# Kernel optimization log

Measured on AMD Instinct MI355X. Metric: run time of the kernel, lower is better.

The kernel has to match this reference:

```python
import jax, jax.numpy as jnp
import numpy as np

N_HEAD, D_K, D_V, D_MODEL = 16, 64, 64, 1024
B, S = 2, 2048


def setup_inputs() -> dict:
    key = jax.random.key(0)
    ks = jax.random.split(key, 9)
    Q = jax.random.normal(ks[0], (B, S, D_MODEL), jnp.float32)
    K = jax.random.normal(ks[1], (B, S, D_MODEL), jnp.float32)
    V = jax.random.normal(ks[2], (B, S, D_MODEL), jnp.float32)
    mask = jax.random.randint(ks[3], (B, 1, S), 0, 2) > 0  # bool, ~half valid
    # xavier-normal-ish std for (d_model, d_k) fan
    std_qk = (2.0 / (D_MODEL + D_K)) ** 0.5
    std_v = (2.0 / (D_MODEL + D_V)) ** 0.5
    Wq = std_qk * jax.random.normal(ks[4], (N_HEAD, D_MODEL, D_K), jnp.float32)
    Wk = std_qk * jax.random.normal(ks[5], (N_HEAD, D_MODEL, D_K), jnp.float32)
    Wv = std_v * jax.random.normal(ks[6], (N_HEAD, D_MODEL, D_V), jnp.float32)
    bound = (6.0 / (N_HEAD * D_V)) ** 0.5  # kaiming_uniform-ish
    Wo = jax.random.uniform(ks[7], (N_HEAD * D_V, D_MODEL), jnp.float32, -bound, bound)
    return {"Q": Q, "K": K, "V": V, "Wq": Wq, "Wk": Wk, "Wv": Wv, "Wo": Wo, "mask": mask}


def reference(Q, K, V, Wq, Wk, Wv, Wo, mask):
    n_head, d_model, d_k = Wq.shape
    d_v = Wv.shape[-1]
    b, sq, _ = Q.shape
    sk = K.shape[1]
    # Per-head projections; torch cat over heads == leading head axis here.
    q = jnp.einsum('bsd,hdk->hbsk', Q, Wq)  # (H,B,Sq,dk)
    k = jnp.einsum('bsd,hdk->hbsk', K, Wk)  # (H,B,Sk,dk)
    v = jnp.einsum('bsd,hdv->hbsv', V, Wv)  # (H,B,Sk,dv)
    scores = jnp.einsum('hbqk,hbsk->hbqs', q, k) / (d_k ** 0.5)
    m = mask[None]  # (1,B,1,Sk), broadcasts over heads and queries
    scores = jnp.where(m, scores, -1e9)
    attn = jax.nn.softmax(scores, axis=-1)
    attn = jnp.where(m, attn, 0.0)
    out = jnp.einsum('hbqs,hbsv->hbqv', attn, v)  # (H,B,Sq,dv)
    # torch: split along batch*head dim then cat on feature dim -> head-major feature concat
    out = jnp.transpose(out, (1, 2, 0, 3)).reshape(b, sq, n_head * d_v)
    out = out @ Wo  # (B,Sq,d_model); dropout is identity in eval
    attns = attn.reshape(n_head * b, sq, sk)
    return out, attns
```

## Files before the change

### kernel.cpp

```cpp
#include <hip/hip_runtime.h>
#include <hip/hip_bf16.h>

typedef __attribute__((ext_vector_type(8))) short short8;
typedef __attribute__((ext_vector_type(4))) float floatx4;

#define H 16
#define BB 2
#define SS 2048
#define DM 1024
#define DK 64

__device__ __forceinline__ unsigned short f2bf(float f) {
  union { float f; unsigned int u; } x; x.f = f;
  unsigned int r = (x.u + 0x7fffu + ((x.u >> 16) & 1u)) >> 16;
  return (unsigned short)r;
}
__device__ __forceinline__ float bf2f(unsigned short h) {
  union { unsigned int u; float f; } x; x.u = (unsigned int)h << 16;
  return x.f;
}

__global__ __launch_bounds__(256) void convert_qkv(
    const float* __restrict__ Q, const float* __restrict__ K, const float* __restrict__ V,
    unsigned short* __restrict__ Qb, unsigned short* __restrict__ Kb,
    unsigned short* __restrict__ Vb) {
  const float* in; unsigned short* out;
  int z = blockIdx.y;
  if (z == 0)      { in = Q; out = Qb; }
  else if (z == 1) { in = K; out = Kb; }
  else             { in = V; out = Vb; }
  size_t i = ((size_t)blockIdx.x * 256 + threadIdx.x) * 4;
  float4 v = *(const float4*)&in[i];
  ushort4 o;
  o.x = f2bf(v.x); o.y = f2bf(v.y); o.z = f2bf(v.z); o.w = f2bf(v.w);
  *(ushort4*)&out[i] = o;
}

__global__ __launch_bounds__(256) void repack_w(
    const float* __restrict__ Wq, const float* __restrict__ Wk,
    const float* __restrict__ Wv, const float* __restrict__ Wo,
    unsigned short* __restrict__ Wq_t, unsigned short* __restrict__ Wk_t,
    unsigned short* __restrict__ Wv_t, unsigned short* __restrict__ Wo_t) {
  int z = blockIdx.z;
  int bx = blockIdx.x, by = blockIdx.y;
  int t = threadIdx.x;
  const float* in;
  unsigned short* out;
  if (z == 0)      { in = Wq; out = Wq_t; }
  else if (z == 1) { in = Wk; out = Wk_t; }
  else if (z == 2) { in = Wv; out = Wv_t; }
  else             { in = Wo; out = Wo_t; }
  #pragma unroll
  for (int i = 0; i < 16; i++) {
    int o = t + i * 256;
    int r = o >> 6, cloc = o & 63;
    if (z < 3) {
      out[(bx * 64 + r) * 1024 + by * 64 + cloc] =
          f2bf(in[bx * 65536 + (by * 64 + cloc) * 64 + r]);
    } else {
      out[(bx * 64 + r) * 1024 + by * 64 + cloc] =
          f2bf(in[(by * 64 + cloc) * 1024 + bx * 64 + r]);
    }
  }
}

__global__ __launch_bounds__(256) void gemm_bt(
    const unsigned short* __restrict__ A, const unsigned short* __restrict__ Bt,
    unsigned short* __restrict__ C, float* __restrict__ Cf, int M, int N, int K) {
  __shared__ __align__(16) unsigned short a_lds[128 * 32];
  __shared__ __align__(16) unsigned short b_lds[128 * 32];
  const int bn = blockIdx.x * 128, bm = blockIdx.y * 128;
  const int t = threadIdx.x;
  const int wave = t >> 6, lane = t & 63;
  const int quad = lane >> 4, l15 = lane & 15;
  const int wm = (wave & 1) * 64, wn = (wave >> 1) * 64;
  floatx4 acc[4][4] = {};
  for (int kt = 0; kt < K; kt += 32) {
    __syncthreads();
    {
      int c = t;
      #pragma unroll
      for (int it = 0; it < 2; it++, c += 256) {
        int row = c >> 2, col = (c & 3) * 8;
        *(uint4*)&a_lds[row * 32 + col] =
            *(const uint4*)&A[(size_t)(bm + row) * K + kt + col];
      }
      c = t;
      #pragma unroll
      for (int it = 0; it < 2; it++, c += 256) {
        int row = c >> 2, col = (c & 3) * 8;
        *(uint4*)&b_lds[row * 32 + col] =
            *(const uint4*)&Bt[(size_t)(bn + row) * K + kt + col];
      }
    }
    __syncthreads();
    short8 af[4], bfr[4];
    #pragma unroll
    for (int mt = 0; mt < 4; mt++)
      af[mt] = *(const short8*)&a_lds[(wm + mt * 16 + l15) * 32 + quad * 8];
    #pragma unroll
    for (int nt = 0; nt < 4; nt++)
      bfr[nt] = *(const short8*)&b_lds[(wn + nt * 16 + l15) * 32 + quad * 8];
    #pragma unroll
    for (int mt = 0; mt < 4; mt++)
      #pragma unroll
      for (int nt = 0; nt < 4; nt++)
        acc[mt][nt] = __builtin_amdgcn_mfma_f32_16x16x32_bf16(af[mt], bfr[nt], acc[mt][nt], 0, 0, 0);
  }
  if (Cf) {
    #pragma unroll
    for (int mt = 0; mt < 4; mt++)
      #pragma unroll
      for (int nt = 0; nt < 4; nt++)
        #pragma unroll
        for (int r = 0; r < 4; r++) {
          int row = bm + wm + mt * 16 + quad * 4 + r;
          int col = bn + wn + nt * 16 + l15;
          Cf[(size_t)row * N + col] = acc[mt][nt][r];
        }
  } else {
    #pragma unroll
    for (int mt = 0; mt < 4; mt++)
      #pragma unroll
      for (int nt = 0; nt < 4; nt++)
        #pragma unroll
        for (int r = 0; r < 4; r++) {
          int row = bm + wm + mt * 16 + quad * 4 + r;
          int col = bn + wn + nt * 16 + l15;
          C[(size_t)row * N + col] = f2bf(acc[mt][nt][r]);
        }
  }
}

__global__ __launch_bounds__(256) void attn_kernel(
    const unsigned short* __restrict__ q2, const unsigned short* __restrict__ k2,
    const unsigned short* __restrict__ vt, const void* __restrict__ mask,
    float* __restrict__ attns, unsigned short* __restrict__ ctx) {
  __shared__ __align__(16) unsigned short k_lds[128 * 64];
  __shared__ __align__(16) unsigned short vt_lds[64 * 128];
  __shared__ __align__(16) unsigned short pq_lds[64 * 128];
  __shared__ float maskmul[SS];
  __shared__ float rowsum_inv[64];
  __shared__ int s_fp32, s_byte2, s_gt1;
  const int qt = blockIdx.x, b = blockIdx.y, h = blockIdx.z;
  const int t = threadIdx.x;
  const int wave = t >> 6, lane = t & 63;
  const int quad = lane >> 4, l15 = lane & 15;

  if (t == 0) { s_fp32 = 1; s_byte2 = 0; s_gt1 = 0; }
  __syncthreads();
  {
    const unsigned int* mw = (const unsigned int*)mask;
    int f_fp32 = 1, f_byte2 = 0, f_gt1 = 0;
    for (int i = t; i < 1024; i += 256) {
      unsigned int w = mw[i];
      if (!(w == 0u || w == 0x3F800000u)) f_fp32 = 0;
      if (((w & 0xFFu) > 1u) || (((w >> 8) & 0xFFu) > 1u) ||
          (((w >> 16) & 0xFFu) > 1u) || ((w >> 24) > 1u)) f_byte2 = 1;
      if (w > 1u) f_gt1 = 1;
    }
    if (!f_fp32) atomicAnd(&s_fp32, 0);
    if (f_byte2) atomicOr(&s_byte2, 1);
    if (f_gt1)  atomicOr(&s_gt1, 1);
  }
  __syncthreads();
  {
    const unsigned int*   mw = (const unsigned int*)mask;
    const unsigned short* mh = (const unsigned short*)mask;
    const unsigned char*  mb = (const unsigned char*)mask;
    int mode = s_fp32 ? 0 : (s_byte2 ? 1 : (s_gt1 ? 2 : 3));
    for (int i = t; i < SS; i += 256) {
      int idx = b * SS + i;
      bool mv;
      if (mode == 0)      mv = mw[idx] != 0u;
      else if (mode == 1) mv = mh[idx] != 0u;
      else if (mode == 2) mv = mb[idx] != 0u;
      else                mv = mw[idx] != 0u;
      maskmul[i] = mv ? 1.0f : 0.0f;
    }
  }

  {
    int c = t;
    #pragma unroll
    for (int it = 0; it < 2; it++, c += 256) {
      int r = c >> 3, cc = (c & 7) * 8;
      *(uint4*)&pq_lds[r * 64 + cc] =
          *(const uint4*)&q2[(size_t)(b * SS + qt * 64 + r) * DM + h * DK + cc];
    }
  }
  __syncthreads();
  short8 aq0 = *(const short8*)&pq_lds[(wave * 16 + l15) * 64 + quad * 8];
  short8 aq1 = *(const short8*)&pq_lds[(wave * 16 + l15) * 64 + 32 + quad * 8];

  const float cexp = 0.18033688011112042f;
  float rs[4] = {0.f, 0.f, 0.f, 0.f};

  for (int kt = 0; kt < 16; kt++) {
    __syncthreads();
    int c = t;
    #pragma unroll
    for (int it = 0; it < 4; it++, c += 256) {
      int r = c >> 3, cc = (c & 7) * 8;
      *(uint4*)&k_lds[r * 64 + cc] =
          *(const uint4*)&k2[(size_t)(b * SS + kt * 128 + r) * DM + h * DK + cc];
    }
    __syncthreads();
    #pragma unroll
    for (int ct = 0; ct < 8; ct++) {
      floatx4 s = {};
      short8 bk0 = *(const short8*)&k_lds[(ct * 16 + l15) * 64 + quad * 8];
      short8 bk1 = *(const short8*)&k_lds[(ct * 16 + l15) * 64 + 32 + quad * 8];
      s = __builtin_amdgcn_mfma_f32_16x16x32_bf16(aq0, bk0, s, 0, 0, 0);
      s = __builtin_amdgcn_mfma_f32_16x16x32_bf16(aq1, bk1, s, 0, 0, 0);
      float m = maskmul[kt * 128 + ct * 16 + l15];
      #pragma unroll
      for (int r = 0; r < 4; r++) rs[r] += m * exp2f(s[r] * cexp);
    }
  }
  #pragma unroll
  for (int r = 0; r < 4; r++) {
    rs[r] += __shfl_xor(rs[r], 1);
    rs[r] += __shfl_xor(rs[r], 2);
    rs[r] += __shfl_xor(rs[r], 4);
    rs[r] += __shfl_xor(rs[r], 8);
  }
  if (l15 == 0) {
    #pragma unroll
    for (int r = 0; r < 4; r++)
      rowsum_inv[wave * 16 + quad * 4 + r] = rs[r] > 0.f ? 1.0f / rs[r] : 0.f;
  }

  floatx4 cacc[4] = {};
  for (int kt = 0; kt < 16; kt++) {
    __syncthreads();
    {
      int c = t;
      #pragma unroll
      for (int it = 0; it < 4; it++, c += 256) {
        int r = c >> 3, cc = (c & 7) * 8;
        *(uint4*)&k_lds[r * 64 + cc] =
            *(const uint4*)&k2[(size_t)(b * SS + kt * 128 + r) * DM + h * DK + cc];
      }
      c = t;
      #pragma unroll
      for (int it = 0; it < 4; it++, c += 256) {
        int n = c >> 4, cc = (c & 15) * 8;
        *(uint4*)&vt_lds[n * 128 + cc] =
            *(const uint4*)&vt[(size_t)(h * DK + n) * (BB * SS) + b * SS + kt * 128 + cc];
      }
    }
    __syncthreads();
    float rinv[4];
    #pragma unroll
    for (int r = 0; r < 4; r++) rinv[r] = rowsum_inv[wave * 16 + quad * 4 + r];
    #pragma unroll
    for (int ct = 0; ct < 8; ct++) {
      floatx4 s = {};
      short8 bk0 = *(const short8*)&k_lds[(ct * 16 + l15) * 64 + quad * 8];
      short8 bk1 = *(const short8*)&k_lds[(ct * 16 + l15) * 64 + 32 + quad * 8];
      s = __builtin_amdgcn_mfma_f32_16x16x32_bf16(aq0, bk0, s, 0, 0, 0);
      s = __builtin_amdgcn_mfma_f32_16x16x32_bf16(aq1, bk1, s, 0, 0, 0);
      float m = maskmul[kt * 128 + ct * 16 + l15];
      #pragma unroll
      for (int r = 0; r < 4; r++) {
        float p = m * exp2f(s[r] * cexp) * rinv[r];
        pq_lds[(wave * 16 + quad * 4 + r) * 128 + ct * 16 + l15] = f2bf(p);
      }
    }
    __syncthreads();
    {
      int c = t;
      #pragma unroll
      for (int it = 0; it < 8; it++, c += 256) {
        int r = c >> 5, fc = (c & 31) * 4;
        const unsigned short* src = &pq_lds[r * 128 + fc];
        float4 f;
        f.x = bf2f(src[0]); f.y = bf2f(src[1]);
        f.z = bf2f(src[2]); f.w = bf2f(src[3]);
        *(float4*)&attns[((size_t)(h * BB + b) * SS + qt * 64 + r) * SS + kt * 128 + fc] = f;
      }
    }
    #pragma unroll
    for (int ks = 0; ks < 4; ks++) {
      short8 ap = *(const short8*)&pq_lds[(wave * 16 + l15) * 128 + ks * 32 + quad * 8];
      #pragma unroll
      for (int ct = 0; ct < 4; ct++) {
        short8 bv = *(const short8*)&vt_lds[(ct * 16 + l15) * 128 + ks * 32 + quad * 8];
        cacc[ct] = __builtin_amdgcn_mfma_f32_16x16x32_bf16(ap, bv, cacc[ct], 0, 0, 0);
      }
    }
  }
  #pragma unroll
  for (int ct = 0; ct < 4; ct++)
    #pragma unroll
    for (int r = 0; r < 4; r++) {
      int row = b * SS + qt * 64 + wave * 16 + quad * 4 + r;
      int col = h * DK + ct * 16 + l15;
      ctx[(size_t)row * DM + col] = f2bf(cacc[ct][r]);
    }
}

extern "C" void kernel_launch(void* const* d_in, const int* in_sizes, int n_in,
                              void* d_out, int out_size, void* d_ws, size_t ws_size,
                              hipStream_t stream) {
  (void)in_sizes; (void)n_in; (void)out_size; (void)ws_size;
  const float* Q  = (const float*)d_in[0];
  const float* K  = (const float*)d_in[1];
  const float* V  = (const float*)d_in[2];
  const float* Wq = (const float*)d_in[3];
  const float* Wk = (const float*)d_in[4];
  const float* Wv = (const float*)d_in[5];
  const float* Wo = (const float*)d_in[6];
  const void* mask = d_in[7];

  float* out   = (float*)d_out;
  float* attns = out + (size_t)BB * SS * DM;

  char* ws = (char*)d_ws;
  unsigned short* Qb   = (unsigned short*)(ws);
  unsigned short* Kb   = (unsigned short*)(ws + (size_t)(8u  << 20));
  unsigned short* Vb   = (unsigned short*)(ws + (size_t)(16u << 20));
  unsigned short* q2   = (unsigned short*)(ws + (size_t)(24u << 20));
  unsigned short* k2   = (unsigned short*)(ws + (size_t)(32u << 20));
  unsigned short* vt   = (unsigned short*)(ws + (size_t)(40u << 20));
  unsigned short* ctx  = (unsigned short*)(ws + (size_t)(48u << 20));
  unsigned short* Wq_t = (unsigned short*)(ws + (size_t)(56u << 20));
  unsigned short* Wk_t = (unsigned short*)(ws + (size_t)(58u << 20));
  unsigned short* Wv_t = (unsigned short*)(ws + (size_t)(60u << 20));
  unsigned short* Wo_t = (unsigned short*)(ws + (size_t)(62u << 20));

  convert_qkv<<<dim3(4096, 3), 256, 0, stream>>>(Q, K, V, Qb, Kb, Vb);
  repack_w<<<dim3(16, 16, 4), 256, 0, stream>>>(Wq, Wk, Wv, Wo, Wq_t, Wk_t, Wv_t, Wo_t);
  gemm_bt<<<dim3(8, 32), 256, 0, stream>>>(Qb, Wq_t, q2, nullptr, 4096, 1024, 1024);
  gemm_bt<<<dim3(8, 32), 256, 0, stream>>>(Kb, Wk_t, k2, nullptr, 4096, 1024, 1024);
  gemm_bt<<<dim3(32, 8), 256, 0, stream>>>(Wv_t, Vb, vt, nullptr, 1024, 4096, 1024);
  attn_kernel<<<dim3(32, 2, 16), 256, 0, stream>>>(q2, k2, vt, mask, attns, ctx);
  gemm_bt<<<dim3(8, 32), 256, 0, stream>>>(ctx, Wo_t, nullptr, out, 4096, 1024, 1024);
}
```

Baseline: 880.4 us.

## Shrink GEMM and attention tiles, use direct global-to-LDS loads, pad LDS rows

The GEMM tile drops from 128x128 to 128x64, which doubles the grid, and its operands are loaded with global_load_lds straight into LDS instead of passing through registers. The attention kernel moves from 128-key to 64-key tiles and pads LDS rows to 72 elements to avoid bank conflicts. The mask is stored as bytes, the row inverse-sum is loaded once outside the loop, and the attns copy uses vector LDS reads. The aim is higher occupancy through smaller LDS and register footprints, at the cost of more barriers and loop iterations.

```diff
diff --git a/kernel.cpp b/kernel.cpp
--- a/kernel.cpp
+++ b/kernel.cpp
@@ -18,6 +18,11 @@
 __device__ __forceinline__ float bf2f(unsigned short h) {
   union { unsigned int u; float f; } x; x.u = (unsigned int)h << 16;
   return x.f;
+}
+__device__ __forceinline__ void gld16(const unsigned short* g, unsigned short* l) {
+  __builtin_amdgcn_global_load_lds(
+      (const __attribute__((address_space(1))) unsigned int*)(g),
+      (__attribute__((address_space(3))) unsigned int*)(l), 16, 0, 0);
 }
 
 __global__ __launch_bounds__(256) void convert_qkv(
@@ -68,50 +73,38 @@
     const unsigned short* __restrict__ A, const unsigned short* __restrict__ Bt,
     unsigned short* __restrict__ C, float* __restrict__ Cf, int M, int N, int K) {
   __shared__ __align__(16) unsigned short a_lds[128 * 32];
-  __shared__ __align__(16) unsigned short b_lds[128 * 32];
-  const int bn = blockIdx.x * 128, bm = blockIdx.y * 128;
+  __shared__ __align__(16) unsigned short b_lds[64 * 32];
+  const int bn = blockIdx.x * 64, bm = blockIdx.y * 128;
   const int t = threadIdx.x;
   const int wave = t >> 6, lane = t & 63;
   const int quad = lane >> 4, l15 = lane & 15;
-  const int wm = (wave & 1) * 64, wn = (wave >> 1) * 64;
-  floatx4 acc[4][4] = {};
+  const int wm = (wave & 1) * 64, wn = (wave >> 1) * 32;
+  const int ar0 = t >> 2, ak0 = (t & 3) * 8;
+  floatx4 acc[4][2] = {};
   for (int kt = 0; kt < K; kt += 32) {
     __syncthreads();
-    {
-      int c = t;
-      #pragma unroll
-      for (int it = 0; it < 2; it++, c += 256) {
-        int row = c >> 2, col = (c & 3) * 8;
-        *(uint4*)&a_lds[row * 32 + col] =
-            *(const uint4*)&A[(size_t)(bm + row) * K + kt + col];
-      }
-      c = t;
-      #pragma unroll
-      for (int it = 0; it < 2; it++, c += 256) {
-        int row = c >> 2, col = (c & 3) * 8;
-        *(uint4*)&b_lds[row * 32 + col] =
-            *(const uint4*)&Bt[(size_t)(bn + row) * K + kt + col];
-      }
-    }
-    __syncthreads();
-    short8 af[4], bfr[4];
+    gld16(&A[(size_t)(bm + ar0) * K + kt + ak0], &a_lds[t * 8]);
+    gld16(&A[(size_t)(bm + 64 + ar0) * K + kt + ak0], &a_lds[(256 + t) * 8]);
+    gld16(&Bt[(size_t)(bn + ar0) * K + kt + ak0], &b_lds[t * 8]);
+    __syncthreads();
+    short8 af[4], bfr[2];
     #pragma unroll
     for (int mt = 0; mt < 4; mt++)
       af[mt] = *(const short8*)&a_lds[(wm + mt * 16 + l15) * 32 + quad * 8];
     #pragma unroll
-    for (int nt = 0; nt < 4; nt++)
+    for (int nt = 0; nt < 2; nt++)
       bfr[nt] = *(const short8*)&b_lds[(wn + nt * 16 + l15) * 32 + quad * 8];
     #pragma unroll
     for (int mt = 0; mt < 4; mt++)
       #pragma unroll
-      for (int nt = 0; nt < 4; nt++)
+      for (int nt = 0; nt < 2; nt++)
         acc[mt][nt] = __builtin_amdgcn_mfma_f32_16x16x32_bf16(af[mt], bfr[nt], acc[mt][nt], 0, 0, 0);
   }
   if (Cf) {
     #pragma unroll
     for (int mt = 0; mt < 4; mt++)
       #pragma unroll
-      for (int nt = 0; nt < 4; nt++)
+      for (int nt = 0; nt < 2; nt++)
         #pragma unroll
         for (int r = 0; r < 4; r++) {
           int row = bm + wm + mt * 16 + quad * 4 + r;
@@ -122,7 +115,7 @@
     #pragma unroll
     for (int mt = 0; mt < 4; mt++)
       #pragma unroll
-      for (int nt = 0; nt < 4; nt++)
+      for (int nt = 0; nt < 2; nt++)
         #pragma unroll
         for (int r = 0; r < 4; r++) {
           int row = bm + wm + mt * 16 + quad * 4 + r;
@@ -136,10 +129,10 @@
     const unsigned short* __restrict__ q2, const unsigned short* __restrict__ k2,
     const unsigned short* __restrict__ vt, const void* __restrict__ mask,
     float* __restrict__ attns, unsigned short* __restrict__ ctx) {
-  __shared__ __align__(16) unsigned short k_lds[128 * 64];
-  __shared__ __align__(16) unsigned short vt_lds[64 * 128];
-  __shared__ __align__(16) unsigned short pq_lds[64 * 128];
-  __shared__ float maskmul[SS];
+  __shared__ __align__(16) unsigned short k_lds[64 * 72];
+  __shared__ __align__(16) unsigned short vt_lds[64 * 72];
+  __shared__ __align__(16) unsigned short pq_lds[64 * 72];
+  __shared__ unsigned char masku8[SS];
   __shared__ float rowsum_inv[64];
   __shared__ int s_fp32, s_byte2, s_gt1;
   const int qt = blockIdx.x, b = blockIdx.y, h = blockIdx.z;
@@ -176,7 +169,7 @@
       else if (mode == 1) mv = mh[idx] != 0u;
       else if (mode == 2) mv = mb[idx] != 0u;
       else                mv = mw[idx] != 0u;
-      maskmul[i] = mv ? 1.0f : 0.0f;
+      masku8[i] = mv ? 1 : 0;
     }
   }
 
@@ -185,35 +178,37 @@
     #pragma unroll
     for (int it = 0; it < 2; it++, c += 256) {
       int r = c >> 3, cc = (c & 7) * 8;
-      *(uint4*)&pq_lds[r * 64 + cc] =
+      *(uint4*)&pq_lds[r * 72 + cc] =
           *(const uint4*)&q2[(size_t)(b * SS + qt * 64 + r) * DM + h * DK + cc];
     }
   }
   __syncthreads();
-  short8 aq0 = *(const short8*)&pq_lds[(wave * 16 + l15) * 64 + quad * 8];
-  short8 aq1 = *(const short8*)&pq_lds[(wave * 16 + l15) * 64 + 32 + quad * 8];
+  short8 aq0 = *(const short8*)&pq_lds[(wave * 16 + l15) * 72 + quad * 8];
+  short8 aq1 = *(const short8*)&pq_lds[(wave * 16 + l15) * 72 + 32 + quad * 8];
 
   const float cexp = 0.18033688011112042f;
   float rs[4] = {0.f, 0.f, 0.f, 0.f};
 
-  for (int kt = 0; kt < 16; kt++) {
-    __syncthreads();
-    int c = t;
-    #pragma unroll
-    for (int it = 0; it < 4; it++, c += 256) {
-      int r = c >> 3, cc = (c & 7) * 8;
-      *(uint4*)&k_lds[r * 64 + cc] =
-          *(const uint4*)&k2[(size_t)(b * SS + kt * 128 + r) * DM + h * DK + cc];
-    }
-    __syncthreads();
-    #pragma unroll
-    for (int ct = 0; ct < 8; ct++) {
+  for (int kt = 0; kt < 32; kt++) {
+    __syncthreads();
+    {
+      int c = t;
+      #pragma unroll
+      for (int it = 0; it < 2; it++, c += 256) {
+        int r = c >> 3, cc = (c & 7) * 8;
+        *(uint4*)&k_lds[r * 72 + cc] =
+            *(const uint4*)&k2[(size_t)(b * SS + kt * 64 + r) * DM + h * DK + cc];
+      }
+    }
+    __syncthreads();
+    #pragma unroll
+    for (int ct = 0; ct < 4; ct++) {
       floatx4 s = {};
-      short8 bk0 = *(const short8*)&k_lds[(ct * 16 + l15) * 64 + quad * 8];
-      short8 bk1 = *(const short8*)&k_lds[(ct * 16 + l15) * 64 + 32 + quad * 8];
+      short8 bk0 = *(const short8*)&k_lds[(ct * 16 + l15) * 72 + quad * 8];
+      short8 bk1 = *(const short8*)&k_lds[(ct * 16 + l15) * 72 + 32 + quad * 8];
       s = __builtin_amdgcn_mfma_f32_16x16x32_bf16(aq0, bk0, s, 0, 0, 0);
       s = __builtin_amdgcn_mfma_f32_16x16x32_bf16(aq1, bk1, s, 0, 0, 0);
-      float m = maskmul[kt * 128 + ct * 16 + l15];
+      float m = (float)masku8[kt * 64 + ct * 16 + l15];
       #pragma unroll
       for (int r = 0; r < 4; r++) rs[r] += m * exp2f(s[r] * cexp);
     }
@@ -230,63 +225,66 @@
     for (int r = 0; r < 4; r++)
       rowsum_inv[wave * 16 + quad * 4 + r] = rs[r] > 0.f ? 1.0f / rs[r] : 0.f;
   }
+  __syncthreads();
+  float rinv[4];
+  #pragma unroll
+  for (int r = 0; r < 4; r++) rinv[r] = rowsum_inv[wave * 16 + quad * 4 + r];
 
   floatx4 cacc[4] = {};
-  for (int kt = 0; kt < 16; kt++) {
+  const size_t attn_base = ((size_t)(h * BB + b) * SS + qt * 64) * SS;
+
+  for (int kt = 0; kt < 32; kt++) {
     __syncthreads();
     {
       int c = t;
       #pragma unroll
-      for (int it = 0; it < 4; it++, c += 256) {
+      for (int it = 0; it < 2; it++, c += 256) {
         int r = c >> 3, cc = (c & 7) * 8;
-        *(uint4*)&k_lds[r * 64 + cc] =
-            *(const uint4*)&k2[(size_t)(b * SS + kt * 128 + r) * DM + h * DK + cc];
+        *(uint4*)&k_lds[r * 72 + cc] =
+            *(const uint4*)&k2[(size_t)(b * SS + kt * 64 + r) * DM + h * DK + cc];
       }
       c = t;
       #pragma unroll
-      for (int it = 0; it < 4; it++, c += 256) {
-        int n = c >> 4, cc = (c & 15) * 8;
-        *(uint4*)&vt_lds[n * 128 + cc] =
-            *(const uint4*)&vt[(size_t)(h * DK + n) * (BB * SS) + b * SS + kt * 128 + cc];
-      }
-    }
-    __syncthreads();
-    float rinv[4];
-    #pragma unroll
-    for (int r = 0; r < 4; r++) rinv[r] = rowsum_inv[wave * 16 + quad * 4 + r];
-    #pragma unroll
-    for (int ct = 0; ct < 8; ct++) {
+      for (int it = 0; it < 2; it++, c += 256) {
+        int n = c >> 3, cc = (c & 7) * 8;
+        *(uint4*)&vt_lds[n * 72 + cc] =
+            *(const uint4*)&vt[(size_t)(h * DK + n) * (BB * SS) + b * SS + kt * 64 + cc];
+      }
+    }
+    __syncthreads();
+    #pragma unroll
+    for (int ct = 0; ct < 4; ct++) {
       floatx4 s = {};
-      short8 bk0 = *(const short8*)&k_lds[(ct * 16 + l15) * 64 + quad * 8];
-      short8 bk1 = *(const short8*)&k_lds[(ct * 16 + l15) * 64 + 32 + quad * 8];
+      short8 bk0 = *(const short8*)&k_lds[(ct * 16 + l15) * 72 + quad * 8];
+      short8 bk1 = *(const short8*)&k_lds[(ct * 16 + l15) * 72 + 32 + quad * 8];
       s = __builtin_amdgcn_mfma_f32_16x16x32_bf16(aq0, bk0, s, 0, 0, 0);
       s = __builtin_amdgcn_mfma_f32_16x16x32_bf16(aq1, bk1, s, 0, 0, 0);
-      float m = maskmul[kt * 128 + ct * 16 + l15];
+      float m = (float)masku8[kt * 64 + ct * 16 + l15];
       #pragma unroll
       for (int r = 0; r < 4; r++) {
         float p = m * exp2f(s[r] * cexp) * rinv[r];
-        pq_lds[(wave * 16 + quad * 4 + r) * 128 + ct * 16 + l15] = f2bf(p);
+        pq_lds[(wave * 16 + quad * 4 + r) * 72 + ct * 16 + l15] = f2bf(p);
       }
     }
     __syncthreads();
     {
       int c = t;
       #pragma unroll
-      for (int it = 0; it < 8; it++, c += 256) {
-        int r = c >> 5, fc = (c & 31) * 4;
-        const unsigned short* src = &pq_lds[r * 128 + fc];
+      for (int it = 0; it < 4; it++, c += 256) {
+        int r = c >> 4, fc = (c & 15) * 4;
+        ushort4 u = *(const ushort4*)&pq_lds[r * 72 + fc];
         float4 f;
-        f.x = bf2f(src[0]); f.y = bf2f(src[1]);
-        f.z = bf2f(src[2]); f.w = bf2f(src[3]);
-        *(float4*)&attns[((size_t)(h * BB + b) * SS + qt * 64 + r) * SS + kt * 128 + fc] = f;
-      }
-    }
-    #pragma unroll
-    for (int ks = 0; ks < 4; ks++) {
-      short8 ap = *(const short8*)&pq_lds[(wave * 16 + l15) * 128 + ks * 32 + quad * 8];
+        f.x = bf2f(u.x); f.y = bf2f(u.y);
+        f.z = bf2f(u.z); f.w = bf2f(u.w);
+        *(float4*)&attns[attn_base + (size_t)r * SS + kt * 64 + fc] = f;
+      }
+    }
+    #pragma unroll
+    for (int ks = 0; ks < 2; ks++) {
+      short8 ap = *(const short8*)&pq_lds[(wave * 16 + l15) * 72 + ks * 32 + quad * 8];
       #pragma unroll
       for (int ct = 0; ct < 4; ct++) {
-        short8 bv = *(const short8*)&vt_lds[(ct * 16 + l15) * 128 + ks * 32 + quad * 8];
+        short8 bv = *(const short8*)&vt_lds[(ct * 16 + l15) * 72 + ks * 32 + quad * 8];
         cacc[ct] = __builtin_amdgcn_mfma_f32_16x16x32_bf16(ap, bv, cacc[ct], 0, 0, 0);
       }
     }
@@ -332,9 +330,9 @@
 
   convert_qkv<<<dim3(4096, 3), 256, 0, stream>>>(Q, K, V, Qb, Kb, Vb);
   repack_w<<<dim3(16, 16, 4), 256, 0, stream>>>(Wq, Wk, Wv, Wo, Wq_t, Wk_t, Wv_t, Wo_t);
-  gemm_bt<<<dim3(8, 32), 256, 0, stream>>>(Qb, Wq_t, q2, nullptr, 4096, 1024, 1024);
-  gemm_bt<<<dim3(8, 32), 256, 0, stream>>>(Kb, Wk_t, k2, nullptr, 4096, 1024, 1024);
-  gemm_bt<<<dim3(32, 8), 256, 0, stream>>>(Wv_t, Vb, vt, nullptr, 1024, 4096, 1024);
+  gemm_bt<<<dim3(16, 32), 256, 0, stream>>>(Qb, Wq_t, q2, nullptr, 4096, 1024, 1024);
+  gemm_bt<<<dim3(16, 32), 256, 0, stream>>>(Kb, Wk_t, k2, nullptr, 4096, 1024, 1024);
+  gemm_bt<<<dim3(64, 8), 256, 0, stream>>>(Wv_t, Vb, vt, nullptr, 1024, 4096, 1024);
   attn_kernel<<<dim3(32, 2, 16), 256, 0, stream>>>(q2, k2, vt, mask, attns, ctx);
-  gemm_bt<<<dim3(8, 32), 256, 0, stream>>>(ctx, Wo_t, nullptr, out, 4096, 1024, 1024);
-}
+  gemm_bt<<<dim3(16, 32), 256, 0, stream>>>(ctx, Wo_t, nullptr, out, 4096, 1024, 1024);
+}
```

Measured after the change: 831.5 us. 1.06x faster.
